# Kernel tuning notes

Hardware: AMD Instinct MI355X
Metric: run time of the kernel (lower is better)

Reference implementation:

```python
import jax, jax.numpy as jnp
import numpy as np

N = 50000
E = 1600000
F_IN = 128
C_OUT = 64
HEADS = 2
NEG_SLOPE = 0.2
EPS = 1e-5


def setup_inputs() -> dict:
    key = jax.random.key(0)
    ks = jax.random.split(key, 8)
    HC = HEADS * C_OUT
    glorot = lambda k, shape: jax.random.normal(k, shape, jnp.float32) * np.sqrt(2.0 / (shape[0] + shape[-1]))
    return {
        "x": jax.random.normal(ks[0], (N, F_IN), jnp.float32),
        "edge_index": jax.random.randint(ks[1], (2, E), 0, N, jnp.int64),
        "W_l": glorot(ks[2], (F_IN, HC)),
        "W_r": glorot(ks[3], (F_IN, HC)),
        "att": glorot(ks[4], (HEADS, C_OUT)),
        "bias": jnp.zeros((HC,), jnp.float32),
        "gn_weight": jnp.ones((HC,), jnp.float32),
        "gn_bias": jnp.zeros((HC,), jnp.float32),
        "gn_mean_scale": jnp.ones((HC,), jnp.float32),
    }


def reference(x, edge_index, W_l, W_r, att, bias, gn_weight, gn_bias, gn_mean_scale):
    n = x.shape[0]
    # --- GATv2Conv (share_weights=False, concat=True, dropout=0) ---
    x_l = (x @ W_l).reshape(n, HEADS, C_OUT)  # source transform
    x_r = (x @ W_r).reshape(n, HEADS, C_OUT)  # target transform
    # add self loops
    loop = jnp.arange(n, dtype=edge_index.dtype)
    src = jnp.concatenate([edge_index[0], loop])
    dst = jnp.concatenate([edge_index[1], loop])
    # edge-wise attention logits: LeakyReLU(x_l[j] + x_r[i]) . att
    xs = x_l[src] + x_r[dst]  # [E', H, C]
    e = jax.nn.leaky_relu(xs, NEG_SLOPE)
    logits = jnp.einsum('ehc,hc->eh', e, att)  # [E', H]
    # segment softmax over edges sharing the same target node
    seg_max = jax.ops.segment_max(logits, dst, num_segments=n)  # [N, H]
    exp = jnp.exp(logits - seg_max[dst])
    seg_sum = jax.ops.segment_sum(exp, dst, num_segments=n)
    alpha = exp / seg_sum[dst]  # [E', H]
    # scatter-aggregate messages
    msg = alpha[:, :, None] * x_l[src]  # [E', H, C]
    out = jax.ops.segment_sum(msg, dst, num_segments=n)  # [N, H, C]
    out = out.reshape(n, HEADS * C_OUT) + bias
    # --- GraphNorm (single graph) ---
    mean = out.mean(axis=0)
    centered = out - mean * gn_mean_scale
    var = (centered * centered).mean(axis=0)
    return gn_weight * centered / jnp.sqrt(var + EPS) + gn_bias
```

## Files before the change

kernel.cpp:

```cpp
#include <hip/hip_runtime.h>
#include <math.h>

#define NEG_SLOPE 0.2f
#define GN_EPS 1e-5f
#define NBSHIFT 8
#define CHUNK 8192

typedef _Float16 h2 __attribute__((ext_vector_type(2)));

__device__ __forceinline__ int rfl(int v) {
  return __builtin_amdgcn_readfirstlane(v);
}

__device__ __forceinline__ unsigned int pkh(float a, float b) {
  return __builtin_bit_cast(unsigned int, __builtin_amdgcn_cvt_pkrtz(a, b));
}

__device__ __forceinline__ h2 bch2(unsigned int u) {
  return __builtin_bit_cast(h2, u);
}

__device__ __forceinline__ h2 mkh2(float a, float b) {
  return __builtin_bit_cast(h2, __builtin_amdgcn_cvt_pkrtz(a, b));
}

__device__ __forceinline__ float dot2f(h2 a, h2 b, float c) {
#if __has_builtin(__builtin_amdgcn_fdot2)
  return __builtin_amdgcn_fdot2(a, b, c, false);
#else
  return fmaf((float)a.x, (float)b.x, fmaf((float)a.y, (float)b.y, c));
#endif
}

__device__ __forceinline__ float lkdot(h2 xl, h2 xr, h2 a, float p) {
  h2 t = xl + xr;
  h2 z = {(_Float16)0.f, (_Float16)0.f};
#if __has_builtin(__builtin_elementwise_min)
  h2 mn = __builtin_elementwise_min(t, z);
#else
  h2 mn;
  mn.x = (t.x < z.x) ? t.x : z.x;
  mn.y = (t.y < z.y) ? t.y : z.y;
#endif
  h2 km1 = {(_Float16)(NEG_SLOPE - 1.0f), (_Float16)(NEG_SLOPE - 1.0f)};
  h2 g = mn * km1 + t;
  return dot2f(g, a, p);
}

__global__ __launch_bounds__(256) void gemm_xw(
    const float* __restrict__ x, const float* __restrict__ Wl,
    const float* __restrict__ Wr, unsigned int* __restrict__ xlb,
    unsigned int* __restrict__ xrh, int n) {
  __shared__ float xs[32][128];
  const int tid = threadIdx.x;
  const int r0 = blockIdx.x * 32;
  const int rows = min(32, n - r0);

#pragma unroll
  for (int j = 0; j < 4; ++j) {
    int f4 = j * 256 + tid;
    int row = f4 >> 5;
    int c4 = f4 & 31;
    float4 v = make_float4(0.f, 0.f, 0.f, 0.f);
    if (row < rows) v = ((const float4*)(x + (size_t)(r0 + row) * 128))[c4];
    ((float4*)&xs[row][0])[c4] = v;
  }
  __syncthreads();

  const int rg = tid >> 6;
  const int cg = tid & 63;
  const float* __restrict__ W = (cg < 32) ? Wl : Wr;
  const int cb = (cg < 32) ? 4 * cg : 4 * cg - 128;

  float4 acc[8];
#pragma unroll
  for (int r = 0; r < 8; ++r) acc[r] = make_float4(0.f, 0.f, 0.f, 0.f);

#pragma unroll 4
  for (int k4 = 0; k4 < 32; ++k4) {
    float4 xv[8];
#pragma unroll
    for (int r = 0; r < 8; ++r)
      xv[r] = *(const float4*)&xs[rg * 8 + r][k4 * 4];
    float4 w0 = *(const float4*)(W + (size_t)(4 * k4 + 0) * 128 + cb);
    float4 w1 = *(const float4*)(W + (size_t)(4 * k4 + 1) * 128 + cb);
    float4 w2 = *(const float4*)(W + (size_t)(4 * k4 + 2) * 128 + cb);
    float4 w3 = *(const float4*)(W + (size_t)(4 * k4 + 3) * 128 + cb);
#pragma unroll
    for (int r = 0; r < 8; ++r) {
      acc[r].x = fmaf(xv[r].x, w0.x, acc[r].x);
      acc[r].y = fmaf(xv[r].x, w0.y, acc[r].y);
      acc[r].z = fmaf(xv[r].x, w0.z, acc[r].z);
      acc[r].w = fmaf(xv[r].x, w0.w, acc[r].w);
      acc[r].x = fmaf(xv[r].y, w1.x, acc[r].x);
      acc[r].y = fmaf(xv[r].y, w1.y, acc[r].y);
      acc[r].z = fmaf(xv[r].y, w1.z, acc[r].z);
      acc[r].w = fmaf(xv[r].y, w1.w, acc[r].w);
      acc[r].x = fmaf(xv[r].z, w2.x, acc[r].x);
      acc[r].y = fmaf(xv[r].z, w2.y, acc[r].y);
      acc[r].z = fmaf(xv[r].z, w2.z, acc[r].z);
      acc[r].w = fmaf(xv[r].z, w2.w, acc[r].w);
      acc[r].x = fmaf(xv[r].w, w3.x, acc[r].x);
      acc[r].y = fmaf(xv[r].w, w3.y, acc[r].y);
      acc[r].z = fmaf(xv[r].w, w3.z, acc[r].z);
      acc[r].w = fmaf(xv[r].w, w3.w, acc[r].w);
    }
  }

  unsigned int* __restrict__ dst = (cg < 32) ? xlb : xrh;
#pragma unroll
  for (int r = 0; r < 8; ++r) {
    int row = rg * 8 + r;
    if (row < rows) {
      uint2 p;
      p.x = pkh(acc[r].x, acc[r].y);
      p.y = pkh(acc[r].z, acc[r].w);
      *(uint2*)(dst + (size_t)(r0 + row) * 64 + (cb >> 1)) = p;
    }
  }
}

__global__ __launch_bounds__(256) void coarse_hist(const int* __restrict__ ei,
                                                   int* __restrict__ bhist,
                                                   int e) {
  __shared__ int hist[256];
  hist[threadIdx.x] = 0;
  __syncthreads();
  const int stride = gridDim.x * 256;
  for (int i = blockIdx.x * 256 + threadIdx.x; i < e; i += stride)
    atomicAdd(&hist[ei[e + i] >> NBSHIFT], 1);
  __syncthreads();
  int v = hist[threadIdx.x];
  if (v > 0) atomicAdd(&bhist[threadIdx.x], v);
}

__global__ __launch_bounds__(256) void bscan(const int* __restrict__ bhist,
                                             int* __restrict__ bbase,
                                             int* __restrict__ gcur,
                                             int* __restrict__ offsets, int nb,
                                             int n, int e) {
  __shared__ int sd[256];
  int t = threadIdx.x;
  int v = (t < nb) ? bhist[t] : 0;
  sd[t] = v;
  __syncthreads();
#pragma unroll
  for (int s = 1; s < 256; s <<= 1) {
    int add = (t >= s) ? sd[t - s] : 0;
    __syncthreads();
    sd[t] += add;
    __syncthreads();
  }
  int excl = sd[t] - v;
  if (t < nb) {
    bbase[t] = excl;
    gcur[t] = excl;
  } else {
    gcur[t] = 0;
  }
  if (t == 0) {
    bbase[nb] = e;
    offsets[n] = e;
  }
}

__global__ __launch_bounds__(256) void partition(const int* __restrict__ ei,
                                                 int* __restrict__ gcur,
                                                 unsigned int* __restrict__ ebuf,
                                                 int e) {
  __shared__ int hist[256];
  __shared__ int lcur[256];
  const int t = threadIdx.x;
  const int c0 = blockIdx.x * CHUNK;
  const int cend = min(c0 + CHUNK, e);
  hist[t] = 0;
  __syncthreads();
  for (int i = c0 + t; i < cend; i += 256)
    atomicAdd(&hist[ei[e + i] >> NBSHIFT], 1);
  __syncthreads();
  lcur[t] = atomicAdd(&gcur[t], hist[t]);
  __syncthreads();
  for (int i = c0 + t; i < cend; i += 256) {
    int dst = ei[e + i];
    int src = ei[i];
    int b = dst >> NBSHIFT;
    int pos = atomicAdd(&lcur[b], 1);
    ebuf[pos] = (unsigned int)src | ((unsigned int)(dst & 255) << 16);
  }
}

__global__ __launch_bounds__(256) void csr_build(
    const unsigned int* __restrict__ ebuf, const int* __restrict__ bbase,
    int* __restrict__ offsets, int* __restrict__ csr_src, int n) {
  __shared__ int hist[256];
  __shared__ int sc[256];
  const int b = blockIdx.x;
  const int t = threadIdx.x;
  const int node0 = b << NBSHIFT;
  const int seg0 = bbase[b];
  const int seg1 = bbase[b + 1];

  hist[t] = 0;
  __syncthreads();
  for (int i = seg0 + t; i < seg1; i += 256)
    atomicAdd(&hist[(ebuf[i] >> 16) & 255], 1);
  __syncthreads();
  int v = hist[t];
  sc[t] = v;
  __syncthreads();
#pragma unroll
  for (int s = 1; s < 256; s <<= 1) {
    int add = (t >= s) ? sc[t - s] : 0;
    __syncthreads();
    sc[t] += add;
    __syncthreads();
  }
  int start = seg0 + sc[t] - v;
  int node = node0 + t;
  if (node < n) offsets[node] = start;
  __syncthreads();
  hist[t] = start;
  __syncthreads();
  for (int i = seg0 + t; i < seg1; i += 256) {
    unsigned int u = ebuf[i];
    int pos = atomicAdd(&hist[(u >> 16) & 255], 1);
    csr_src[pos] = (int)(u & 0xFFFFu);
  }
}

__global__ __launch_bounds__(256) void node_agg(
    const unsigned int* __restrict__ xlh, const unsigned int* __restrict__ xrh,
    const int* __restrict__ offsets, const int* __restrict__ csr_src,
    const float* __restrict__ att, const float* __restrict__ bias,
    float* __restrict__ out, int n) {
  const int wave = threadIdx.x >> 6;
  const int lane = threadIdx.x & 63;
  const int node = blockIdx.x * 4 + wave;
  if (node >= n) return;
  const int q = lane >> 4;
  const int r = lane & 15;

  const uint4 xr4 = *(const uint4*)(xrh + (size_t)node * 64 + r * 4);
  const h2 xr0 = bch2(xr4.x), xr1 = bch2(xr4.y), xr2v = bch2(xr4.z),
           xr3 = bch2(xr4.w);
  const float4 a0 = *(const float4*)(att + r * 8);
  const float4 a1 = *(const float4*)(att + r * 8 + 4);
  const h2 ah0 = mkh2(a0.x, a0.y), ah1 = mkh2(a0.z, a0.w),
           ah2 = mkh2(a1.x, a1.y), ah3 = mkh2(a1.z, a1.w);

  const int start = rfl(offsets[node]);
  const int end = rfl(offsets[node + 1]);
  const int deg = end - start;
  const int T = deg + 1;

  float s = 0.f;
  float accf[8];
#pragma unroll
  for (int i = 0; i < 8; ++i) accf[i] = 0.f;

  const unsigned int* __restrict__ xlp = xlh + r * 4;

  for (int b0 = 0; b0 < T; b0 += 64) {
    const int m = min(64, T - b0);
    const int kk = b0 + lane;
    const int cl = min(kk, T - 1);
    int idx = node;
    if (deg > 0) {
      idx = csr_src[start + max(cl - 1, 0)];
      if (cl == 0) idx = node;
    }
#pragma unroll 4
    for (int j = 0; j < m; j += 4) {
      const int eo = j + q;
      const bool valid = eo < m;
      const int src = __shfl(idx, min(eo, m - 1), 64);
      const uint4 xl4 = *(const uint4*)(xlp + (size_t)src * 64);
      const h2 x0 = bch2(xl4.x), x1 = bch2(xl4.y), x2 = bch2(xl4.z),
               x3 = bch2(xl4.w);
      float p = 0.f;
      p = lkdot(x0, xr0, ah0, p);
      p = lkdot(x1, xr1, ah1, p);
      p = lkdot(x2, xr2v, ah2, p);
      p = lkdot(x3, xr3, ah3, p);
      p += __shfl_xor(p, 1, 64);
      p += __shfl_xor(p, 2, 64);
      p += __shfl_xor(p, 4, 64);
      const float w = valid ? __expf(p) : 0.f;
      s += w;
      accf[0] = fmaf((float)x0.x, w, accf[0]);
      accf[1] = fmaf((float)x0.y, w, accf[1]);
      accf[2] = fmaf((float)x1.x, w, accf[2]);
      accf[3] = fmaf((float)x1.y, w, accf[3]);
      accf[4] = fmaf((float)x2.x, w, accf[4]);
      accf[5] = fmaf((float)x2.y, w, accf[5]);
      accf[6] = fmaf((float)x3.x, w, accf[6]);
      accf[7] = fmaf((float)x3.y, w, accf[7]);
    }
  }

  s += __shfl_xor(s, 16, 64);
  s += __shfl_xor(s, 32, 64);
#pragma unroll
  for (int i = 0; i < 8; ++i) {
    accf[i] += __shfl_xor(accf[i], 16, 64);
    accf[i] += __shfl_xor(accf[i], 32, 64);
  }

  if (q == 0) {
    const float inv = 1.f / s;
    const float4 b0v = *(const float4*)(bias + r * 8);
    const float4 b1v = *(const float4*)(bias + r * 8 + 4);
    float4 o0 = make_float4(fmaf(accf[0], inv, b0v.x), fmaf(accf[1], inv, b0v.y),
                            fmaf(accf[2], inv, b0v.z), fmaf(accf[3], inv, b0v.w));
    float4 o1 = make_float4(fmaf(accf[4], inv, b1v.x), fmaf(accf[5], inv, b1v.y),
                            fmaf(accf[6], inv, b1v.z), fmaf(accf[7], inv, b1v.w));
    *(float4*)(out + (size_t)node * 128 + r * 8) = o0;
    *(float4*)(out + (size_t)node * 128 + r * 8 + 4) = o1;
  }
}

__global__ __launch_bounds__(256) void gn_partial(const float* __restrict__ out,
                                                  float* __restrict__ part,
                                                  int total) {
  float s = 0.f, q = 0.f;
  const int stride = gridDim.x * 256;
  for (int idx = blockIdx.x * 256 + threadIdx.x; idx < total; idx += stride) {
    float v = out[idx];
    s += v;
    q = fmaf(v, v, q);
  }
  __shared__ float sd[256], qd[256];
  sd[threadIdx.x] = s;
  qd[threadIdx.x] = q;
  __syncthreads();
  if (threadIdx.x < 128) {
    part[blockIdx.x * 256 + threadIdx.x] = sd[threadIdx.x] + sd[threadIdx.x + 128];
    part[blockIdx.x * 256 + 128 + threadIdx.x] =
        qd[threadIdx.x] + qd[threadIdx.x + 128];
  }
}

__global__ __launch_bounds__(1024) void gn_final(const float* __restrict__ part,
                                                 const float* __restrict__ gw,
                                                 const float* __restrict__ gb,
                                                 const float* __restrict__ gms,
                                                 float* __restrict__ AB,
                                                 int nblocks, float inv_n) {
  __shared__ float sS[8][128];
  __shared__ float sQ[8][128];
  const int c = threadIdx.x & 127;
  const int sl = threadIdx.x >> 7;
  float S = 0.f, Q = 0.f;
#pragma unroll 4
  for (int b = sl; b < nblocks; b += 8) {
    S += part[b * 256 + c];
    Q += part[b * 256 + 128 + c];
  }
  sS[sl][c] = S;
  sQ[sl][c] = Q;
  __syncthreads();
  if (sl == 0) {
#pragma unroll
    for (int i = 1; i < 8; ++i) {
      S += sS[i][c];
      Q += sQ[i][c];
    }
    float mean = S * inv_n;
    float msc = mean * gms[c];
    float var = Q * inv_n - 2.f * msc * mean + msc * msc;
    float scale = gw[c] * rsqrtf(var + GN_EPS);
    AB[c] = scale;
    AB[128 + c] = gb[c] - scale * msc;
  }
}

__global__ void gn_apply(float* __restrict__ out, const float* __restrict__ AB,
                         int total4) {
  int i = blockIdx.x * blockDim.x + threadIdx.x;
  if (i >= total4) return;
  float4 v = ((float4*)out)[i];
  int c4 = (i & 31) * 4;
  v.x = fmaf(AB[c4 + 0], v.x, AB[128 + c4 + 0]);
  v.y = fmaf(AB[c4 + 1], v.y, AB[128 + c4 + 1]);
  v.z = fmaf(AB[c4 + 2], v.z, AB[128 + c4 + 2]);
  v.w = fmaf(AB[c4 + 3], v.w, AB[128 + c4 + 3]);
  ((float4*)out)[i] = v;
}

extern "C" void kernel_launch(void* const* d_in, const int* in_sizes, int n_in,
                              void* d_out, int out_size, void* d_ws,
                              size_t ws_size, hipStream_t stream) {
  const float* x = (const float*)d_in[0];
  const int* ei = (const int*)d_in[1];
  const float* Wl = (const float*)d_in[2];
  const float* Wr = (const float*)d_in[3];
  const float* att = (const float*)d_in[4];
  const float* bias = (const float*)d_in[5];
  const float* gw = (const float*)d_in[6];
  const float* gb = (const float*)d_in[7];
  const float* gms = (const float*)d_in[8];
  float* out = (float*)d_out;

  const int n = in_sizes[0] / 128;
  const int e = in_sizes[1] / 2;
  const int nb = (n + 255) >> NBSHIFT;
  const int nchunks = (e + CHUNK - 1) / CHUNK;
  const int GN_BLOCKS = 256;

  char* w = (char*)d_ws;
  auto alloc = [&](size_t bytes) {
    char* p = w;
    w += (bytes + 255) & ~(size_t)255;
    return p;
  };
  unsigned int* xlb = (unsigned int*)alloc((size_t)n * 64 * sizeof(int));
  unsigned int* xrh = (unsigned int*)alloc((size_t)n * 64 * sizeof(int));
  int* offsets = (int*)alloc((size_t)(n + 1) * sizeof(int));
  int* csr_src = (int*)alloc((size_t)e * sizeof(int));
  unsigned int* ebuf = (unsigned int*)alloc((size_t)e * sizeof(int));
  int* bhist = (int*)alloc(256 * sizeof(int));
  int* bbase = (int*)alloc((size_t)(nb + 1) * sizeof(int));
  int* gcur = (int*)alloc(256 * sizeof(int));
  float* part = (float*)alloc((size_t)GN_BLOCKS * 256 * sizeof(float));
  float* AB = (float*)alloc(256 * sizeof(float));

  hipMemsetAsync(bhist, 0, 256 * sizeof(int), stream);

  gemm_xw<<<(n + 31) / 32, 256, 0, stream>>>(x, Wl, Wr, xlb, xrh, n);
  coarse_hist<<<196, 256, 0, stream>>>(ei, bhist, e);
  bscan<<<1, 256, 0, stream>>>(bhist, bbase, gcur, offsets, nb, n, e);
  partition<<<nchunks, 256, 0, stream>>>(ei, gcur, ebuf, e);
  csr_build<<<nb, 256, 0, stream>>>(ebuf, bbase, offsets, csr_src, n);
  node_agg<<<(n + 3) / 4, 256, 0, stream>>>(xlb, xrh, offsets, csr_src, att,
                                            bias, out, n);
  gn_partial<<<GN_BLOCKS, 256, 0, stream>>>(out, part, n * 128);
  gn_final<<<1, 1024, 0, stream>>>(part, gw, gb, gms, AB, GN_BLOCKS,
                                   1.0f / (float)n);
  gn_apply<<<(n * 32 + 255) / 256, 256, 0, stream>>>(out, AB, n * 32);
}
```

Before: 294.9 us.

## Use MFMA fp16 for feature GEMM, fuse with histogram, split aggregation tail

The scalar fp32 shared-memory GEMM is replaced by an MFMA 16x16x32 fp16 GEMM that loads W and x directly from global memory and converts them to half on the fly. The coarse destination histogram is folded into the same launch as extra blocks, which removes one kernel launch and lets the two run concurrently. The node aggregation loop is split into a full-quad main loop without validity checks and a single masked tail. Converting x and W to fp16 before the multiply lowers input precision, and it drops the LDS staging of x.

```diff
diff --git a/kernel.cpp b/kernel.cpp
--- a/kernel.cpp
+++ b/kernel.cpp
@@ -7,6 +7,8 @@
 #define CHUNK 8192
 
 typedef _Float16 h2 __attribute__((ext_vector_type(2)));
+typedef _Float16 half8 __attribute__((ext_vector_type(8)));
+typedef float f32x4 __attribute__((ext_vector_type(4)));
 
 __device__ __forceinline__ int rfl(int v) {
   return __builtin_amdgcn_readfirstlane(v);
@@ -47,91 +49,97 @@
   return dot2f(g, a, p);
 }
 
-__global__ __launch_bounds__(256) void gemm_xw(
+__global__ __launch_bounds__(256) void gemm_hist(
     const float* __restrict__ x, const float* __restrict__ Wl,
     const float* __restrict__ Wr, unsigned int* __restrict__ xlb,
-    unsigned int* __restrict__ xrh, int n) {
-  __shared__ float xs[32][128];
-  const int tid = threadIdx.x;
-  const int r0 = blockIdx.x * 32;
-  const int rows = min(32, n - r0);
-
-#pragma unroll
-  for (int j = 0; j < 4; ++j) {
-    int f4 = j * 256 + tid;
-    int row = f4 >> 5;
-    int c4 = f4 & 31;
-    float4 v = make_float4(0.f, 0.f, 0.f, 0.f);
-    if (row < rows) v = ((const float4*)(x + (size_t)(r0 + row) * 128))[c4];
-    ((float4*)&xs[row][0])[c4] = v;
-  }
-  __syncthreads();
-
-  const int rg = tid >> 6;
-  const int cg = tid & 63;
-  const float* __restrict__ W = (cg < 32) ? Wl : Wr;
-  const int cb = (cg < 32) ? 4 * cg : 4 * cg - 128;
-
-  float4 acc[8];
-#pragma unroll
-  for (int r = 0; r < 8; ++r) acc[r] = make_float4(0.f, 0.f, 0.f, 0.f);
-
-#pragma unroll 4
-  for (int k4 = 0; k4 < 32; ++k4) {
-    float4 xv[8];
-#pragma unroll
-    for (int r = 0; r < 8; ++r)
-      xv[r] = *(const float4*)&xs[rg * 8 + r][k4 * 4];
-    float4 w0 = *(const float4*)(W + (size_t)(4 * k4 + 0) * 128 + cb);
-    float4 w1 = *(const float4*)(W + (size_t)(4 * k4 + 1) * 128 + cb);
-    float4 w2 = *(const float4*)(W + (size_t)(4 * k4 + 2) * 128 + cb);
-    float4 w3 = *(const float4*)(W + (size_t)(4 * k4 + 3) * 128 + cb);
-#pragma unroll
-    for (int r = 0; r < 8; ++r) {
-      acc[r].x = fmaf(xv[r].x, w0.x, acc[r].x);
-      acc[r].y = fmaf(xv[r].x, w0.y, acc[r].y);
-      acc[r].z = fmaf(xv[r].x, w0.z, acc[r].z);
-      acc[r].w = fmaf(xv[r].x, w0.w, acc[r].w);
-      acc[r].x = fmaf(xv[r].y, w1.x, acc[r].x);
-      acc[r].y = fmaf(xv[r].y, w1.y, acc[r].y);
-      acc[r].z = fmaf(xv[r].y, w1.z, acc[r].z);
-      acc[r].w = fmaf(xv[r].y, w1.w, acc[r].w);
-      acc[r].x = fmaf(xv[r].z, w2.x, acc[r].x);
-      acc[r].y = fmaf(xv[r].z, w2.y, acc[r].y);
-      acc[r].z = fmaf(xv[r].z, w2.z, acc[r].z);
-      acc[r].w = fmaf(xv[r].z, w2.w, acc[r].w);
-      acc[r].x = fmaf(xv[r].w, w3.x, acc[r].x);
-      acc[r].y = fmaf(xv[r].w, w3.y, acc[r].y);
-      acc[r].z = fmaf(xv[r].w, w3.z, acc[r].z);
-      acc[r].w = fmaf(xv[r].w, w3.w, acc[r].w);
-    }
-  }
-
-  unsigned int* __restrict__ dst = (cg < 32) ? xlb : xrh;
-#pragma unroll
-  for (int r = 0; r < 8; ++r) {
-    int row = rg * 8 + r;
-    if (row < rows) {
+    unsigned int* __restrict__ xrh, int n, const int* __restrict__ ei,
+    int* __restrict__ bhist, int e, int gemm_blocks) {
+  if ((int)blockIdx.x >= gemm_blocks) {
+    __shared__ int hist[256];
+    hist[threadIdx.x] = 0;
+    __syncthreads();
+    const int nbk = gridDim.x - gemm_blocks;
+    const int stride = nbk * 256;
+    for (int i = ((int)blockIdx.x - gemm_blocks) * 256 + threadIdx.x; i < e;
+         i += stride)
+      atomicAdd(&hist[ei[e + i] >> NBSHIFT], 1);
+    __syncthreads();
+    int v = hist[threadIdx.x];
+    if (v > 0) atomicAdd(&bhist[threadIdx.x], v);
+    return;
+  }
+
+  const int wv = threadIdx.x >> 6;
+  const int lane = threadIdx.x & 63;
+  const int lr = lane & 15;
+  const int lk = lane >> 4;
+  const int node0 = (int)blockIdx.x * 64;
+  const float* __restrict__ Wp = (wv < 2) ? Wl : Wr;
+  unsigned int* __restrict__ dst = (wv < 2) ? xlb : xrh;
+  const int chBase = (wv & 1) * 64;
+
+  f32x4 acc[4][4];
+#pragma unroll
+  for (int mt = 0; mt < 4; ++mt)
+#pragma unroll
+    for (int nt = 0; nt < 4; ++nt) acc[mt][nt] = (f32x4){0.f, 0.f, 0.f, 0.f};
+
+  int nd[4];
+#pragma unroll
+  for (int nt = 0; nt < 4; ++nt) nd[nt] = min(node0 + nt * 16 + lr, n - 1);
+
+#pragma unroll
+  for (int kc = 0; kc < 4; ++kc) {
+    const int k0 = kc * 32 + lk * 8;
+    half8 a[4];
+#pragma unroll
+    for (int mt = 0; mt < 4; ++mt) {
+      const float* __restrict__ wp =
+          Wp + (size_t)k0 * 128 + chBase + mt * 16 + lr;
+      float w0 = wp[0 * 128], w1 = wp[1 * 128], w2 = wp[2 * 128],
+            w3 = wp[3 * 128];
+      float w4 = wp[4 * 128], w5 = wp[5 * 128], w6 = wp[6 * 128],
+            w7 = wp[7 * 128];
+      uint4 ua;
+      ua.x = pkh(w0, w1);
+      ua.y = pkh(w2, w3);
+      ua.z = pkh(w4, w5);
+      ua.w = pkh(w6, w7);
+      a[mt] = __builtin_bit_cast(half8, ua);
+    }
+    half8 b[4];
+#pragma unroll
+    for (int nt = 0; nt < 4; ++nt) {
+      const float4 f0 = *(const float4*)(x + (size_t)nd[nt] * 128 + k0);
+      const float4 f1 = *(const float4*)(x + (size_t)nd[nt] * 128 + k0 + 4);
+      uint4 ub;
+      ub.x = pkh(f0.x, f0.y);
+      ub.y = pkh(f0.z, f0.w);
+      ub.z = pkh(f1.x, f1.y);
+      ub.w = pkh(f1.z, f1.w);
+      b[nt] = __builtin_bit_cast(half8, ub);
+    }
+#pragma unroll
+    for (int mt = 0; mt < 4; ++mt)
+#pragma unroll
+      for (int nt = 0; nt < 4; ++nt)
+        acc[mt][nt] = __builtin_amdgcn_mfma_f32_16x16x32_f16(
+            a[mt], b[nt], acc[mt][nt], 0, 0, 0);
+  }
+
+  const int dw0 = (chBase >> 1) + lk * 2;
+#pragma unroll
+  for (int nt = 0; nt < 4; ++nt) {
+    const int node = node0 + nt * 16 + lr;
+    if (node >= n) continue;
+#pragma unroll
+    for (int mt = 0; mt < 4; ++mt) {
       uint2 p;
-      p.x = pkh(acc[r].x, acc[r].y);
-      p.y = pkh(acc[r].z, acc[r].w);
-      *(uint2*)(dst + (size_t)(r0 + row) * 64 + (cb >> 1)) = p;
-    }
-  }
-}
-
-__global__ __launch_bounds__(256) void coarse_hist(const int* __restrict__ ei,
-                                                   int* __restrict__ bhist,
-                                                   int e) {
-  __shared__ int hist[256];
-  hist[threadIdx.x] = 0;
-  __syncthreads();
-  const int stride = gridDim.x * 256;
-  for (int i = blockIdx.x * 256 + threadIdx.x; i < e; i += stride)
-    atomicAdd(&hist[ei[e + i] >> NBSHIFT], 1);
-  __syncthreads();
-  int v = hist[threadIdx.x];
-  if (v > 0) atomicAdd(&bhist[threadIdx.x], v);
+      p.x = pkh(acc[mt][nt][0], acc[mt][nt][1]);
+      p.y = pkh(acc[mt][nt][2], acc[mt][nt][3]);
+      *(uint2*)(dst + (size_t)node * 64 + dw0 + mt * 8) = p;
+    }
+  }
 }
 
 __global__ __launch_bounds__(256) void bscan(const int* __restrict__ bhist,
@@ -260,6 +268,30 @@
 
   const unsigned int* __restrict__ xlp = xlh + r * 4;
 
+  auto quad = [&](int src, bool valid) {
+    const uint4 xl4 = *(const uint4*)(xlp + (size_t)src * 64);
+    const h2 x0 = bch2(xl4.x), x1 = bch2(xl4.y), x2 = bch2(xl4.z),
+             x3 = bch2(xl4.w);
+    float p = 0.f;
+    p = lkdot(x0, xr0, ah0, p);
+    p = lkdot(x1, xr1, ah1, p);
+    p = lkdot(x2, xr2v, ah2, p);
+    p = lkdot(x3, xr3, ah3, p);
+    p += __shfl_xor(p, 1, 64);
+    p += __shfl_xor(p, 2, 64);
+    p += __shfl_xor(p, 4, 64);
+    const float w = valid ? __expf(p) : 0.f;
+    s += w;
+    accf[0] = fmaf((float)x0.x, w, accf[0]);
+    accf[1] = fmaf((float)x0.y, w, accf[1]);
+    accf[2] = fmaf((float)x1.x, w, accf[2]);
+    accf[3] = fmaf((float)x1.y, w, accf[3]);
+    accf[4] = fmaf((float)x2.x, w, accf[4]);
+    accf[5] = fmaf((float)x2.y, w, accf[5]);
+    accf[6] = fmaf((float)x3.x, w, accf[6]);
+    accf[7] = fmaf((float)x3.y, w, accf[7]);
+  };
+
   for (int b0 = 0; b0 < T; b0 += 64) {
     const int m = min(64, T - b0);
     const int kk = b0 + lane;
@@ -269,32 +301,13 @@
       idx = csr_src[start + max(cl - 1, 0)];
       if (cl == 0) idx = node;
     }
-#pragma unroll 4
-    for (int j = 0; j < m; j += 4) {
+    int j = 0;
+#pragma unroll 2
+    for (; j + 4 <= m; j += 4)
+      quad(__shfl(idx, j + q, 64), true);
+    if (j < m) {
       const int eo = j + q;
-      const bool valid = eo < m;
-      const int src = __shfl(idx, min(eo, m - 1), 64);
-      const uint4 xl4 = *(const uint4*)(xlp + (size_t)src * 64);
-      const h2 x0 = bch2(xl4.x), x1 = bch2(xl4.y), x2 = bch2(xl4.z),
-               x3 = bch2(xl4.w);
-      float p = 0.f;
-      p = lkdot(x0, xr0, ah0, p);
-      p = lkdot(x1, xr1, ah1, p);
-      p = lkdot(x2, xr2v, ah2, p);
-      p = lkdot(x3, xr3, ah3, p);
-      p += __shfl_xor(p, 1, 64);
-      p += __shfl_xor(p, 2, 64);
-      p += __shfl_xor(p, 4, 64);
-      const float w = valid ? __expf(p) : 0.f;
-      s += w;
-      accf[0] = fmaf((float)x0.x, w, accf[0]);
-      accf[1] = fmaf((float)x0.y, w, accf[1]);
-      accf[2] = fmaf((float)x1.x, w, accf[2]);
-      accf[3] = fmaf((float)x1.y, w, accf[3]);
-      accf[4] = fmaf((float)x2.x, w, accf[4]);
-      accf[5] = fmaf((float)x2.y, w, accf[5]);
-      accf[6] = fmaf((float)x3.x, w, accf[6]);
-      accf[7] = fmaf((float)x3.y, w, accf[7]);
+      quad(__shfl(idx, min(eo, m - 1), 64), eo < m);
     }
   }
 
@@ -406,6 +419,8 @@
   const int nb = (n + 255) >> NBSHIFT;
   const int nchunks = (e + CHUNK - 1) / CHUNK;
   const int GN_BLOCKS = 256;
+  const int gemm_blocks = (n + 63) / 64;
+  const int hist_blocks = 196;
 
   char* w = (char*)d_ws;
   auto alloc = [&](size_t bytes) {
@@ -426,8 +441,8 @@
 
   hipMemsetAsync(bhist, 0, 256 * sizeof(int), stream);
 
-  gemm_xw<<<(n + 31) / 32, 256, 0, stream>>>(x, Wl, Wr, xlb, xrh, n);
-  coarse_hist<<<196, 256, 0, stream>>>(ei, bhist, e);
+  gemm_hist<<<gemm_blocks + hist_blocks, 256, 0, stream>>>(
+      x, Wl, Wr, xlb, xrh, n, ei, bhist, e, gemm_blocks);
   bscan<<<1, 256, 0, stream>>>(bhist, bbase, gcur, offsets, nb, n, e);
   partition<<<nchunks, 256, 0, stream>>>(ei, gcur, ebuf, e);
   csr_build<<<nb, 256, 0, stream>>>(ebuf, bbase, offsets, csr_src, n);
```

Measured after the change: 270.0 us. 8.5% less time.
